# Performance work log

Measured on AMD Instinct MI355X. Metric: run time of the kernel, lower is better.

The kernel has to match this reference:

```python
import jax, jax.numpy as jnp
import numpy as np

D_MODEL = 1024
N_HEADS = 16
D_K = D_MODEL // N_HEADS
SEQ = 2048
BATCH = 2
THETA = 10000.0


def _rope(x, token_positions):
    # x: [b, h, s, dk]; token_positions: [s] int
    k = jnp.arange(0, D_K, 2, dtype=jnp.float32)
    freqs = 1.0 / (THETA ** (k / D_K))                    # [dk/2]
    angles = token_positions.astype(jnp.float32)[:, None] * freqs[None, :]  # [s, dk/2]
    cos = jnp.cos(angles)
    sin = jnp.sin(angles)
    x1 = x[..., 0::2]
    x2 = x[..., 1::2]
    r1 = x1 * cos - x2 * sin
    r2 = x1 * sin + x2 * cos
    out = jnp.stack([r1, r2], axis=-1)                    # [b,h,s,dk/2,2]
    return out.reshape(x.shape)


def setup_inputs() -> dict:
    key = jax.random.key(0)
    ks = jax.random.split(key, 5)
    sigma = np.sqrt(2.0 / (D_MODEL + D_MODEL))
    x = jax.random.normal(ks[0], (BATCH, SEQ, D_MODEL), dtype=jnp.float32)
    Wq = jax.random.truncated_normal(ks[1], -3.0, 3.0, (D_MODEL, D_MODEL), dtype=jnp.float32) * sigma
    Wk = jax.random.truncated_normal(ks[2], -3.0, 3.0, (D_MODEL, D_MODEL), dtype=jnp.float32) * sigma
    Wv = jax.random.truncated_normal(ks[3], -3.0, 3.0, (D_MODEL, D_MODEL), dtype=jnp.float32) * sigma
    Wo = jax.random.truncated_normal(ks[4], -3.0, 3.0, (D_MODEL, D_MODEL), dtype=jnp.float32) * sigma
    token_positions = jnp.arange(SEQ, dtype=jnp.int64)
    return {"x": x, "Wq": Wq, "Wk": Wk, "Wv": Wv, "Wo": Wo, "token_positions": token_positions}


def reference(x, Wq, Wk, Wv, Wo, token_positions):
    b, s, d = x.shape
    # projections: Linear stores weight [out,in], applies x @ W.T
    Q = x @ Wq.T
    K = x @ Wk.T
    V = x @ Wv.T
    # [b, s, h*dk] -> [b, h, s, dk]
    def split_heads(t):
        return t.reshape(b, s, N_HEADS, D_K).transpose(0, 2, 1, 3)
    Q, K, V = split_heads(Q), split_heads(K), split_heads(V)
    Q = _rope(Q, token_positions)
    K = _rope(K, token_positions)
    scale = 1.0 / np.sqrt(D_K).astype(np.float32)
    scores = jnp.einsum('bhqd,bhkd->bhqk', Q, K) * scale   # [b,h,s,s]
    causal = jnp.tril(jnp.ones((s, s), dtype=bool))
    scores = jnp.where(causal, scores, -jnp.inf)
    attn = jax.nn.softmax(scores, axis=-1)
    out = jnp.einsum('bhqk,bhkd->bhqd', attn, V)           # [b,h,s,dk]
    out = out.transpose(0, 2, 1, 3).reshape(b, s, d)
    return out @ Wo.T
```

## Files before the change

### kernel.cpp

```cpp
#include <hip/hip_runtime.h>
#include <hip/hip_bf16.h>
#include <stdint.h>

#define SEQL   2048
#define NBATCH 2
#define BSZ    4096
#define DMODEL 1024
#define NH     16
#define DK     64
#define NBH    32
#define NCHUNK_TOT 40

typedef __attribute__((ext_vector_type(8)))  short short8;
typedef __attribute__((ext_vector_type(4)))  short shortx4;
typedef __attribute__((ext_vector_type(4)))  float f32x4;
typedef __attribute__((ext_vector_type(16))) float f32x16;
typedef __attribute__((ext_vector_type(4)))  unsigned uint4v;
union PU { uint4v u; short8 s; };

__device__ __forceinline__ short f2b(float f) {
  unsigned u = __float_as_uint(f);
  u = (u + 0x7FFF + ((u >> 16) & 1)) >> 16;
  return (short)u;
}
__device__ __forceinline__ float b2f(short s) {
  return __uint_as_float(((unsigned)(unsigned short)s) << 16);
}
__device__ __forceinline__ unsigned cvtpk(float lo, float hi) {
  unsigned r;
  asm("v_cvt_pk_bf16_f32 %0, %1, %2" : "=v"(r) : "v"(lo), "v"(hi));
  return r;
}
__device__ __forceinline__ float max3f(float a, float b, float c) {
  float d;
  asm("v_max3_f32 %0, %1, %2, %3" : "=v"(d) : "v"(a), "v"(b), "v"(c));
  return d;
}
#define PLSWAP(a_, b_) asm("v_permlane32_swap_b32 %0, %1" : "+v"(a_), "+v"(b_))

__device__ __forceinline__ void g2l16(const void* g, void* l) {
  __builtin_amdgcn_global_load_lds(
      (__attribute__((address_space(1))) void*)(uintptr_t)g,
      (__attribute__((address_space(3))) void*)l, 16, 0, 0);
}

__device__ __forceinline__ f32x4 mfma16(short8 a, short8 b, f32x4 c) {
  return __builtin_amdgcn_mfma_f32_16x16x32_bf16(a, b, c, 0, 0, 0);
}
__device__ __forceinline__ f32x16 mfma32(short8 a, short8 b, f32x16 c) {
  return __builtin_amdgcn_mfma_f32_32x32x16_bf16(a, b, c, 0, 0, 0);
}

__global__ void cvt_all(const float* __restrict__ x,  const float* __restrict__ wq,
                        const float* __restrict__ wk, const float* __restrict__ wv,
                        const float* __restrict__ wo, short* __restrict__ xb,
                        short* __restrict__ wqkv, short* __restrict__ wob) {
  long idx = ((long)blockIdx.x * 256 + threadIdx.x) * 4;
  const float* s; short* d; long off;
  if (idx < 4194304L)      { s = x;  d = xb;             off = idx; }
  else if (idx < 5242880L) { s = wq; d = wqkv;           off = idx - 4194304L; }
  else if (idx < 6291456L) { s = wk; d = wqkv + 1048576; off = idx - 5242880L; }
  else if (idx < 7340032L) { s = wv; d = wqkv + 2097152; off = idx - 6291456L; }
  else                     { s = wo; d = wob;            off = idx - 7340032L; }
  float4 v = *(const float4*)(s + off);
  shortx4 r;
  r[0] = f2b(v.x); r[1] = f2b(v.y); r[2] = f2b(v.z); r[3] = f2b(v.w);
  *(shortx4*)(d + off) = r;
}

__global__ __launch_bounds__(512, 1)
void gemm256(const short* __restrict__ A, const short* __restrict__ B,
             short* __restrict__ C) {
  __shared__ short As[2][16384];
  __shared__ short Bs[2][12288];
  int id = blockIdx.x;
  int swz = (id & 7) * 32 + (id >> 3);
  int bm = swz >> 4, bn = swz & 15;
  int brow = bm << 8, bcoln = bn * 192;
  int tid = threadIdx.x, w = tid >> 6;
  int wm = w >> 2, wn = w & 3;
  int lr = tid & 15, lg = (tid >> 4) & 3;
  const short* Abase = A + (long)brow * 1024;
  const short* Bbase = B + (long)bcoln * 1024;

  f32x4 acc[8][3];
#pragma unroll
  for (int mi = 0; mi < 8; ++mi)
#pragma unroll
    for (int ni = 0; ni < 3; ++ni) acc[mi][ni] = (f32x4){0.f, 0.f, 0.f, 0.f};

#define STGA(s_, kt_, buf_) do {                                                \
    int r_ = tid >> 3, gch_ = (tid & 7) ^ (r_ & 7);                             \
    g2l16(Abase + (long)((s_) * 64 + r_) * 1024 + (kt_) * 64 + gch_ * 8,        \
          &As[buf_][(s_) * 4096 + tid * 8]); } while (0)
#define STGB(s_, kt_, buf_) do {                                                \
    int r_ = tid >> 3, gch_ = (tid & 7) ^ (r_ & 7);                             \
    g2l16(Bbase + (long)((s_) * 64 + r_) * 1024 + (kt_) * 64 + gch_ * 8,        \
          &Bs[buf_][(s_) * 4096 + tid * 8]); } while (0)

  STGA(0,0,0); STGA(1,0,0); STGA(2,0,0); STGA(3,0,0);
  STGB(0,0,0); STGB(1,0,0); STGB(2,0,0);
  STGA(0,1,1); STGA(1,1,1); STGA(2,1,1); STGA(3,1,1);
  STGB(0,1,1); STGB(1,1,1); STGB(2,1,1);
  asm volatile("s_waitcnt vmcnt(7)" ::: "memory");
  __builtin_amdgcn_s_barrier();

  for (int kt = 0; kt < 16; ++kt) {
    int cur = kt & 1;
    const short* Ah = &As[cur][wm * 8192];
    const short* Bh = &Bs[cur][0];
    short8 a0[4][2], a1[4][2], bf[3][2];
#pragma unroll
    for (int mi = 0; mi < 4; ++mi) {
      int rin = mi * 16 + lr;
#pragma unroll
      for (int ks = 0; ks < 2; ++ks)
        a0[mi][ks] = *(const short8*)
            &Ah[rin * 64 + (((ks * 4 + lg) ^ (rin & 7)) << 3)];
    }
#pragma unroll
    for (int ni = 0; ni < 3; ++ni) {
      int ci = wn * 48 + ni * 16 + lr;
      int sub = ci >> 6, rin = ci & 63;
#pragma unroll
      for (int ks = 0; ks < 2; ++ks)
        bf[ni][ks] = *(const short8*)
            &Bh[sub * 4096 + rin * 64 + (((ks * 4 + lg) ^ (rin & 7)) << 3)];
    }
    asm volatile("s_waitcnt lgkmcnt(0)" ::: "memory");
    __builtin_amdgcn_sched_barrier(0);
    __builtin_amdgcn_s_setprio(1);
#pragma unroll
    for (int mi = 0; mi < 4; ++mi)
#pragma unroll
      for (int ni = 0; ni < 2; ++ni)
#pragma unroll
        for (int ks = 0; ks < 2; ++ks)
          acc[mi][ni] = mfma16(a0[mi][ks], bf[ni][ks], acc[mi][ni]);
    __builtin_amdgcn_s_setprio(0);
    __builtin_amdgcn_s_barrier();
#pragma unroll
    for (int mi = 0; mi < 4; ++mi) {
      int rin = mi * 16 + lr;
#pragma unroll
      for (int ks = 0; ks < 2; ++ks)
        a1[mi][ks] = *(const short8*)
            &Ah[4096 + rin * 64 + (((ks * 4 + lg) ^ (rin & 7)) << 3)];
    }
    __builtin_amdgcn_s_setprio(1);
#pragma unroll
    for (int mi = 0; mi < 4; ++mi)
#pragma unroll
      for (int ks = 0; ks < 2; ++ks)
        acc[mi][2] = mfma16(a0[mi][ks], bf[2][ks], acc[mi][2]);
    __builtin_amdgcn_s_setprio(0);
    asm volatile("s_waitcnt lgkmcnt(0)" ::: "memory");
    __builtin_amdgcn_sched_barrier(0);
    __builtin_amdgcn_s_barrier();
    if (kt + 2 < 16) {
      STGA(0, kt + 2, cur); STGA(1, kt + 2, cur);
      STGA(2, kt + 2, cur); STGA(3, kt + 2, cur);
    }
    __builtin_amdgcn_s_setprio(1);
#pragma unroll
    for (int mi = 0; mi < 4; ++mi)
#pragma unroll
      for (int ni = 0; ni < 2; ++ni)
#pragma unroll
        for (int ks = 0; ks < 2; ++ks)
          acc[mi + 4][ni] = mfma16(a1[mi][ks], bf[ni][ks], acc[mi + 4][ni]);
    __builtin_amdgcn_s_setprio(0);
    __builtin_amdgcn_s_barrier();
    if (kt + 2 < 16) {
      STGB(0, kt + 2, cur); STGB(1, kt + 2, cur); STGB(2, kt + 2, cur);
    }
    __builtin_amdgcn_s_setprio(1);
#pragma unroll
    for (int mi = 0; mi < 4; ++mi)
#pragma unroll
      for (int ks = 0; ks < 2; ++ks)
        acc[mi + 4][2] = mfma16(a1[mi][ks], bf[2][ks], acc[mi + 4][2]);
    __builtin_amdgcn_s_setprio(0);
    if (kt + 1 < 16) {
      if (kt + 2 < 16) asm volatile("s_waitcnt vmcnt(7)" ::: "memory");
      else             asm volatile("s_waitcnt vmcnt(0)" ::: "memory");
    }
    __builtin_amdgcn_s_barrier();
  }
#undef STGA
#undef STGB

#pragma unroll
  for (int mi = 0; mi < 8; ++mi)
#pragma unroll
    for (int ni = 0; ni < 3; ++ni)
#pragma unroll
      for (int rr = 0; rr < 4; ++rr) {
        int grow = brow + wm * 128 + mi * 16 + lg * 4 + rr;
        int gcol = bcoln + wn * 48 + ni * 16 + lr;
        int mat = gcol >> 10, cin = gcol & 1023;
        C[(long)mat * 4194304 + (long)grow * 1024 + cin] = f2b(acc[mi][ni][rr]);
      }
}

template<int CBF16>
__global__ __launch_bounds__(256, 2)
void gemm_bt(const short* __restrict__ A, const short* __restrict__ B,
             void* __restrict__ Cv, int M, int N, int K,
             long bStride, long cStride) {
  __shared__ short As[2][4096];
  __shared__ short Bs[2][4096];
  B += (long)blockIdx.y * bStride;
  int nbn = N >> 7;
  int bm = blockIdx.x / nbn, bn = blockIdx.x % nbn;
  int tid = threadIdx.x, w = tid >> 6, l = tid & 63;
  int wm = w >> 1, wn = w & 1;
  int lr = l & 15, lg = l >> 4;
  int brow = bm << 7, bcol = bn << 7;

  const f32x4 fz = {0.f, 0.f, 0.f, 0.f};
  f32x4 acc[4][4];
#pragma unroll
  for (int xi = 0; xi < 4; ++xi)
#pragma unroll
    for (int yi = 0; yi < 4; ++yi) acc[xi][yi] = fz;

#define GSTAGE(k0_, bi_) do {                                                   \
    _Pragma("unroll")                                                           \
    for (int i_ = 0; i_ < 2; ++i_) {                                            \
      int c_ = w * 2 + i_;                                                      \
      int chunk_ = c_ * 64 + l;                                                 \
      int row_ = chunk_ >> 2, ch_ = chunk_ & 3;                                 \
      int gch_ = ch_ ^ ((row_ >> 1) & 3);                                       \
      g2l16(A + (long)(brow + row_) * K + (k0_) + gch_ * 8, &As[bi_][c_ * 512]);\
      g2l16(B + (long)(bcol + row_) * K + (k0_) + gch_ * 8, &Bs[bi_][c_ * 512]);\
    }                                                                           \
  } while (0)

  GSTAGE(0, 0);
  for (int k0 = 0; k0 < K; k0 += 32) {
    int cb = (k0 >> 5) & 1;
    if (k0 + 32 < K) {
      GSTAGE(k0 + 32, cb ^ 1);
      asm volatile("s_waitcnt vmcnt(4)" ::: "memory");
    } else {
      asm volatile("s_waitcnt vmcnt(0)" ::: "memory");
    }
    __builtin_amdgcn_s_barrier();

    short8 af[4], bfr[4];
#pragma unroll
    for (int xi = 0; xi < 4; ++xi) {
      int ar = wm * 64 + xi * 16 + lr;
      af[xi] = *(const short8*)&As[cb][ar * 32 + ((lg ^ ((ar >> 1) & 3)) << 3)];
      int br = wn * 64 + xi * 16 + lr;
      bfr[xi] = *(const short8*)&Bs[cb][br * 32 + ((lg ^ ((br >> 1) & 3)) << 3)];
    }
    __builtin_amdgcn_s_setprio(1);
#pragma unroll
    for (int xi = 0; xi < 4; ++xi)
#pragma unroll
      for (int yi = 0; yi < 4; ++yi)
        acc[xi][yi] = mfma16(af[xi], bfr[yi], acc[xi][yi]);
    __builtin_amdgcn_s_setprio(0);
    asm volatile("s_waitcnt lgkmcnt(0)" ::: "memory");
    __builtin_amdgcn_s_barrier();
  }
#undef GSTAGE

  if (CBF16) {
    short* Cp = (short*)Cv + (long)blockIdx.y * cStride;
#pragma unroll
    for (int xi = 0; xi < 4; ++xi)
#pragma unroll
      for (int yi = 0; yi < 4; ++yi)
#pragma unroll
        for (int r = 0; r < 4; ++r) {
          int row = brow + wm * 64 + xi * 16 + lg * 4 + r;
          int col = bcol + wn * 64 + yi * 16 + lr;
          Cp[(long)row * N + col] = f2b(acc[xi][yi][r]);
        }
  } else {
    float* Cp = (float*)Cv;
#pragma unroll
    for (int xi = 0; xi < 4; ++xi)
#pragma unroll
      for (int yi = 0; yi < 4; ++yi)
#pragma unroll
        for (int r = 0; r < 4; ++r) {
          int row = brow + wm * 64 + xi * 16 + lg * 4 + r;
          int col = bcol + wn * 64 + yi * 16 + lr;
          Cp[(long)row * N + col] = acc[xi][yi][r];
        }
  }
}

__global__ void rope_split(const short* __restrict__ qkv, const int* __restrict__ tok,
                           short* __restrict__ Qh, short* __restrict__ Kh) {
  int t = blockIdx.x * 256 + threadIdx.x;
  int qd = t & 15, h = (t >> 4) & 15, bs = t >> 8;
  int b = bs >> 11, s = bs & 2047;
  float pos = (float)tok[s];
  long srcoff = (long)bs * 1024 + h * 64 + qd * 4;
  shortx4 q4 = *(const shortx4*)(qkv + srcoff);
  shortx4 k4 = *(const shortx4*)(qkv + 4194304L + srcoff);
  shortx4 qo, ko;
#pragma unroll
  for (int p = 0; p < 2; ++p) {
    int i = qd * 2 + p;
    float freq = exp2f(-(float)i * (13.287712379549449f / 32.0f));
    float ang = pos * freq;
    float sn, cs;
    sincosf(ang, &sn, &cs);
    const float QS = 0.125f * 1.44269504f;
    float x1 = b2f(q4[p * 2]), x2 = b2f(q4[p * 2 + 1]);
    qo[p * 2]     = f2b((x1 * cs - x2 * sn) * QS);
    qo[p * 2 + 1] = f2b((x1 * sn + x2 * cs) * QS);
    float y1 = b2f(k4[p * 2]), y2 = b2f(k4[p * 2 + 1]);
    ko[p * 2]     = f2b(y1 * cs - y2 * sn);
    ko[p * 2 + 1] = f2b(y1 * sn + y2 * cs);
  }
  long outoff = ((long)(b * 16 + h) * 2048 + s) * 64 + qd * 4;
  *(shortx4*)(Qh + outoff) = qo;
  *(shortx4*)(Kh + outoff) = ko;
}

__global__ void vtrans(const short* __restrict__ Vlin, short* __restrict__ Vt) {
  __shared__ short tile[64][72];
  int s0 = blockIdx.x * 64;
  int bh = blockIdx.y;
  int b = bh >> 4, h = bh & 15;
  int t = threadIdx.x;
  int r = t >> 2, c0 = (t & 3) * 16;
  const short* src = Vlin + ((long)(b * 2048 + s0 + r)) * 1024 + h * 64 + c0;
  *(short8*)&tile[r][c0]     = *(const short8*)src;
  *(short8*)&tile[r][c0 + 8] = *(const short8*)(src + 8);
  __syncthreads();
  int d = t >> 2, sc0 = (t & 3) * 16;
  short8 o0, o1;
#pragma unroll
  for (int j = 0; j < 8; ++j) { o0[j] = tile[sc0 + j][d]; o1[j] = tile[sc0 + 8 + j][d]; }
  short* dst = Vt + ((long)(bh * 64 + d)) * 2048 + s0 + sc0;
  *(short8*)dst       = o0;
  *(short8*)(dst + 8) = o1;
}

__global__ __launch_bounds__(256, 4)
void attn_fwd(const short* __restrict__ Qh, const short* __restrict__ Kh,
              const short* __restrict__ Vt, short* __restrict__ poO,
              float* __restrict__ pmb, float* __restrict__ plb) {
  __shared__ short Ks[2][4096];
  __shared__ short Vs[2][4096];
  int bh = blockIdx.x;
  int xr = 39 - blockIdx.y;
  int qi, c = xr, nc = 1;
  for (qi = 0; qi < 16; ++qi) { nc = (qi >> 2) + 1; if (c < nc) break; c -= nc; }
  int n = 2 * qi + 2;
  int t0 = (c * n) / nc, t1 = ((c + 1) * n) / nc;
  int q0b = qi << 7;
  int tid = threadIdx.x, w = tid >> 6, l = tid & 63;
  int ql = l & 31, hi = l >> 5;
  const short* Qb = Qh + (long)bh * (2048 * 64);
  const short* Kb = Kh + (long)bh * (2048 * 64);
  const short* Vb = Vt + (long)bh * (64 * 2048);
  int qw = q0b + 32 * w;
  int qg = qw + ql;
  int pid = bh * NCHUNK_TOT + xr;

  short8 qf[4];
#pragma unroll
  for (int kc = 0; kc < 4; ++kc)
    qf[kc] = *(const short8*)(Qb + (long)qg * 64 + kc * 16 + hi * 8);

  f32x16 o0, o1, rsv;
#pragma unroll
  for (int r = 0; r < 16; ++r) { o0[r] = 0.f; o1[r] = 0.f; rsv[r] = 0.f; }
  float m = -1e30f;

#define STAGE(t_, bufi_) do {                                                   \
    int s0_ = (t_) << 6;                                                        \
    _Pragma("unroll")                                                           \
    for (int i_ = 0; i_ < 2; ++i_) {                                            \
      int c_ = w + 4 * i_;                                                      \
      int g_ = c_ >> 2, cc_ = c_ & 3;                                           \
      g2l16(Kb + ((long)(s0_ + g_ * 32 + ql)) * 64 + cc_ * 16 + hi * 8,         \
            &Ks[bufi_][c_ * 512]);                                              \
      g2l16(Vb + ((long)(g_ * 32 + ql)) * 2048 + s0_ + cc_ * 16 + hi * 8,       \
            &Vs[bufi_][c_ * 512]);                                              \
    }                                                                           \
  } while (0)

  STAGE(t0, 0);

  for (int t = t0; t < t1; ++t) {
    int cur = (t - t0) & 1;
    if (t + 1 < t1) {
      STAGE(t + 1, cur ^ 1);
      asm volatile("s_waitcnt vmcnt(4)" ::: "memory");
    } else {
      asm volatile("s_waitcnt vmcnt(0)" ::: "memory");
    }
    __builtin_amdgcn_s_barrier();
    int s0 = t << 6;
    if (s0 <= qw + 31) {
      bool upper = (s0 + 32 <= qw + 31);
      f32x16 sT0, sT1;
#pragma unroll
      for (int r = 0; r < 16; ++r) { sT0[r] = 0.f; sT1[r] = 0.f; }
      __builtin_amdgcn_s_setprio(1);
#pragma unroll
      for (int kc = 0; kc < 4; ++kc) {
        short8 k0 = *(const short8*)&Ks[cur][(kc * 64 + l) * 8];
        sT0 = mfma32(k0, qf[kc], sT0);
      }
      if (upper) {
#pragma unroll
        for (int kc = 0; kc < 4; ++kc) {
          short8 k1 = *(const short8*)&Ks[cur][((4 + kc) * 64 + l) * 8];
          sT1 = mfma32(k1, qf[kc], sT1);
        }
      }
      __builtin_amdgcn_s_setprio(0);
      if (s0 + 63 > qw) {
#pragma unroll
        for (int r = 0; r < 16; ++r) {
          int kvl = (r & 3) + 8 * (r >> 2) + 4 * hi;
          if (s0 + kvl > qg) sT0[r] = -1e30f;
        }
        if (upper) {
#pragma unroll
          for (int r = 0; r < 16; ++r) {
            int kvl = (r & 3) + 8 * (r >> 2) + 4 * hi;
            if (s0 + 32 + kvl > qg) sT1[r] = -1e30f;
          }
        }
      }
      float pmax = fmaxf(sT0[0], sT0[1]);
#pragma unroll
      for (int r = 2; r < 16; r += 2) pmax = max3f(pmax, sT0[r], sT0[r + 1]);
      if (upper) {
#pragma unroll
        for (int r = 0; r < 16; r += 2) pmax = max3f(pmax, sT1[r], sT1[r + 1]);
      }
      pmax = fmaxf(pmax, __shfl_xor(pmax, 32));
      if (__any(pmax > m + 11.5416f)) {
        float mn = fmaxf(m, pmax);
        float sf = exp2f(m - mn);
        m = mn;
#pragma unroll
        for (int r = 0; r < 16; ++r) rsv[r] *= sf;
#pragma unroll
        for (int r = 0; r < 16; ++r) {
          int row = (r & 3) + 8 * (r >> 2) + 4 * hi;
          float fo = __shfl(sf, row);
          o0[r] *= fo; o1[r] *= fo;
        }
      }
#pragma unroll
      for (int r = 0; r < 16; ++r) {
        float p = exp2f(sT0[r] - m);
        sT0[r] = p; rsv[r] += p;
      }
      if (upper) {
#pragma unroll
        for (int r = 0; r < 16; ++r) {
          float p = exp2f(sT1[r] - m);
          sT1[r] = p; rsv[r] += p;
        }
      }
      short8 pa[4];
      {
        unsigned cA[4], cB[4];
#pragma unroll
        for (int g = 0; g < 4; ++g) {
          cA[g] = cvtpk(sT0[4 * g], sT0[4 * g + 1]);
          cB[g] = cvtpk(sT0[4 * g + 2], sT0[4 * g + 3]);
        }
        PLSWAP(cA[0], cA[1]); PLSWAP(cB[0], cB[1]);
        PLSWAP(cA[2], cA[3]); PLSWAP(cB[2], cB[3]);
        PU p0; p0.u = (uint4v){cA[0], cB[0], cA[1], cB[1]}; pa[0] = p0.s;
        PU p1; p1.u = (uint4v){cA[2], cB[2], cA[3], cB[3]}; pa[1] = p1.s;
      }
      if (upper) {
        unsigned cA[4], cB[4];
#pragma unroll
        for (int g = 0; g < 4; ++g) {
          cA[g] = cvtpk(sT1[4 * g], sT1[4 * g + 1]);
          cB[g] = cvtpk(sT1[4 * g + 2], sT1[4 * g + 3]);
        }
        PLSWAP(cA[0], cA[1]); PLSWAP(cB[0], cB[1]);
        PLSWAP(cA[2], cA[3]); PLSWAP(cB[2], cB[3]);
        PU p2; p2.u = (uint4v){cA[0], cB[0], cA[1], cB[1]}; pa[2] = p2.s;
        PU p3; p3.u = (uint4v){cA[2], cB[2], cA[3], cB[3]}; pa[3] = p3.s;
      }
      __builtin_amdgcn_s_setprio(1);
#pragma unroll
      for (int kc = 0; kc < 2; ++kc) {
        short8 v0 = *(const short8*)&Vs[cur][(kc * 64 + l) * 8];
        short8 v1 = *(const short8*)&Vs[cur][((4 + kc) * 64 + l) * 8];
        o0 = mfma32(pa[kc], v0, o0);
        o1 = mfma32(pa[kc], v1, o1);
      }
      if (upper) {
#pragma unroll
        for (int kc = 2; kc < 4; ++kc) {
          short8 v0 = *(const short8*)&Vs[cur][(kc * 64 + l) * 8];
          short8 v1 = *(const short8*)&Vs[cur][((4 + kc) * 64 + l) * 8];
          o0 = mfma32(pa[kc], v0, o0);
          o1 = mfma32(pa[kc], v1, o1);
        }
      }
      __builtin_amdgcn_s_setprio(0);
    }
    asm volatile("s_waitcnt lgkmcnt(0)" ::: "memory");
    __builtin_amdgcn_s_barrier();
  }
#undef STAGE

  float lsum = 0.f;
#pragma unroll
  for (int r = 0; r < 16; ++r) lsum += rsv[r];
  lsum += __shfl_xor(lsum, 32);

  if (hi == 0) {
    pmb[pid * 128 + w * 32 + ql] = m;
    plb[pid * 128 + w * 32 + ql] = lsum;
  }
#pragma unroll
  for (int r = 0; r < 16; ++r) {
    int row = (r & 3) + 8 * (r >> 2) + 4 * hi;
    long basep = ((long)pid * 128 + w * 32 + row) * 64;
    poO[basep + ql]      = f2b(o0[r]);
    poO[basep + 32 + ql] = f2b(o1[r]);
  }
}

__global__ void attn_combine(const short* __restrict__ poO,
                             const float* __restrict__ pmb,
                             const float* __restrict__ plb,
                             short* __restrict__ Oh) {
  int x = blockIdx.x, bh = blockIdx.y;
  int qi = x >> 2, sub = x & 3;
  int t = threadIdx.x;
  int r = sub * 32 + (t >> 3);
  int d0 = (t & 7) * 8;
  int nc = (qi >> 2) + 1;
  int prefix = 0;
  for (int j = 0; j < qi; ++j) prefix += (j >> 2) + 1;
  int base = bh * NCHUNK_TOT + prefix;
  float M = -1e30f;
  for (int i = 0; i < nc; ++i)
    M = fmaxf(M, pmb[(base + i) * 128 + r]);
  float acc0 = 0, acc1 = 0, acc2 = 0, acc3 = 0, acc4 = 0, acc5 = 0, acc6 = 0, acc7 = 0;
  float den = 0.f;
  for (int i = 0; i < nc; ++i) {
    float wgt = exp2f(pmb[(base + i) * 128 + r] - M);
    den += wgt * plb[(base + i) * 128 + r];
    short8 ov = *(const short8*)&poO[((long)(base + i) * 128 + r) * 64 + d0];
    acc0 += wgt * b2f(ov[0]); acc1 += wgt * b2f(ov[1]);
    acc2 += wgt * b2f(ov[2]); acc3 += wgt * b2f(ov[3]);
    acc4 += wgt * b2f(ov[4]); acc5 += wgt * b2f(ov[5]);
    acc6 += wgt * b2f(ov[6]); acc7 += wgt * b2f(ov[7]);
  }
  float inv = 1.0f / den;
  int b = bh >> 4, h = bh & 15;
  int s = qi * 128 + r;
  short8 out;
  out[0] = f2b(acc0 * inv); out[1] = f2b(acc1 * inv);
  out[2] = f2b(acc2 * inv); out[3] = f2b(acc3 * inv);
  out[4] = f2b(acc4 * inv); out[5] = f2b(acc5 * inv);
  out[6] = f2b(acc6 * inv); out[7] = f2b(acc7 * inv);
  *(short8*)&Oh[((long)(b * 2048 + s)) * 1024 + h * 64 + d0] = out;
}

extern "C" void kernel_launch(void* const* d_in, const int* in_sizes, int n_in,
                              void* d_out, int out_size, void* d_ws, size_t ws_size,
                              hipStream_t stream) {
  const float* x  = (const float*)d_in[0];
  const float* wq = (const float*)d_in[1];
  const float* wk = (const float*)d_in[2];
  const float* wv = (const float*)d_in[3];
  const float* wo = (const float*)d_in[4];
  const int* tok  = (const int*)d_in[5];

  short* wsp  = (short*)d_ws;
  short* xb   = wsp;
  short* wqkv = xb + 4194304;
  short* wob  = wqkv + 3145728;
  short* qkv  = wob + 1048576;
  short* qh   = qkv + 12582912;
  short* kh   = qh + 4194304;
  short* vt   = kh + 4194304;
  short* oh   = vt + 4194304;

  short* poO = qkv;
  float* pmb = (float*)xb;
  float* plb = pmb + NCHUNK_TOT * NBH * 128;

  (void)in_sizes; (void)n_in; (void)out_size; (void)ws_size;

  cvt_all<<<8192, 256, 0, stream>>>(x, wq, wk, wv, wo, xb, wqkv, wob);
  gemm256<<<256, 512, 0, stream>>>(xb, wqkv, qkv);
  rope_split<<<4096, 256, 0, stream>>>(qkv, tok, qh, kh);
  vtrans<<<dim3(32, 32), 256, 0, stream>>>(qkv + 8388608, vt);
  attn_fwd<<<dim3(32, NCHUNK_TOT), 256, 0, stream>>>(qh, kh, vt, poO, pmb, plb);
  attn_combine<<<dim3(64, 32), 256, 0, stream>>>(poO, pmb, plb, oh);
  gemm_bt<0><<<dim3(256, 1), 256, 0, stream>>>(oh, wob, d_out, 4096, 1024, 1024,
                                               0L, 0L);
}
```

Before: 142.3 us.

## Fuse RoPE into QKV GEMM epilogue and triple-buffer attention K/V

Moves the RoPE rotation and Q scaling into the QKV GEMM epilogue, using lane shuffles to pair adjacent columns and hardware sin/cos on range-reduced revolutions, which removes the separate rope_split kernel and its round trip through the intermediate buffer. The attention kernel moves from double to triple buffering of K/V tiles in LDS, with occupancy lowered from 4 to 3 blocks per SM. The row-sum accumulator becomes one scalar per thread, reduced across lanes every tile instead of once at the end, and max3 is replaced by plain fmax. Risks are scattered 2-byte stores to qh/kh in the epilogue, extra transcendental work there, and lower occupancy in attention.

```diff
diff --git a/kernel.cpp b/kernel.cpp
--- a/kernel.cpp
+++ b/kernel.cpp
@@ -30,11 +30,6 @@
   unsigned r;
   asm("v_cvt_pk_bf16_f32 %0, %1, %2" : "=v"(r) : "v"(lo), "v"(hi));
   return r;
-}
-__device__ __forceinline__ float max3f(float a, float b, float c) {
-  float d;
-  asm("v_max3_f32 %0, %1, %2, %3" : "=v"(d) : "v"(a), "v"(b), "v"(c));
-  return d;
 }
 #define PLSWAP(a_, b_) asm("v_permlane32_swap_b32 %0, %1" : "+v"(a_), "+v"(b_))
 
@@ -70,7 +65,8 @@
 
 __global__ __launch_bounds__(512, 1)
 void gemm256(const short* __restrict__ A, const short* __restrict__ B,
-             short* __restrict__ C) {
+             const int* __restrict__ tok, short* __restrict__ qh,
+             short* __restrict__ kh, short* __restrict__ vlin) {
   __shared__ short As[2][16384];
   __shared__ short Bs[2][12288];
   int id = blockIdx.x;
@@ -190,17 +186,46 @@
 #undef STGA
 #undef STGB
 
-#pragma unroll
-  for (int mi = 0; mi < 8; ++mi)
-#pragma unroll
-    for (int ni = 0; ni < 3; ++ni)
-#pragma unroll
-      for (int rr = 0; rr < 4; ++rr) {
-        int grow = brow + wm * 128 + mi * 16 + lg * 4 + rr;
-        int gcol = bcoln + wn * 48 + ni * 16 + lr;
-        int mat = gcol >> 10, cin = gcol & 1023;
-        C[(long)mat * 4194304 + (long)grow * 1024 + cin] = f2b(acc[mi][ni][rr]);
-      }
+  int sbase = brow + wm * 128;
+#pragma unroll
+  for (int ni = 0; ni < 3; ++ni) {
+    int gcol = bcoln + wn * 48 + ni * 16 + lr;
+    int mat = gcol >> 10;
+    int cin = gcol & 1023;
+    if (mat == 2) {
+#pragma unroll
+      for (int mi = 0; mi < 8; ++mi)
+#pragma unroll
+        for (int rr = 0; rr < 4; ++rr) {
+          int grow = sbase + mi * 16 + lg * 4 + rr;
+          vlin[(long)grow * 1024 + cin] = f2b(acc[mi][ni][rr]);
+        }
+    } else {
+      short* dst = mat ? kh : qh;
+      float scale = mat ? 1.0f : 0.125f * 1.44269504f;
+      int d = cin & 63, h = cin >> 6;
+      int i = d >> 1;
+      int odd = d & 1;
+      float frev = exp2f(-(float)i * 0.41524101186f) * 0.15915494309f;
+#pragma unroll
+      for (int mi = 0; mi < 8; ++mi)
+#pragma unroll
+        for (int rr = 0; rr < 4; ++rr) {
+          int grow = sbase + mi * 16 + lg * 4 + rr;
+          int s = grow & 2047, b = grow >> 11;
+          float pos = (float)tok[s];
+          float rev = pos * frev;
+          float fr = rev - floorf(rev);
+          float sn, cs;
+          asm("v_sin_f32 %0, %1" : "=v"(sn) : "v"(fr));
+          asm("v_cos_f32 %0, %1" : "=v"(cs) : "v"(fr));
+          float v = acc[mi][ni][rr];
+          float p = __shfl_xor(v, 1);
+          float out = odd ? (p * sn + v * cs) : (v * cs - p * sn);
+          dst[((long)(b * 16 + h) * 2048 + s) * 64 + d] = f2b(out * scale);
+        }
+    }
+  }
 }
 
 template<int CBF16>
@@ -295,36 +320,6 @@
   }
 }
 
-__global__ void rope_split(const short* __restrict__ qkv, const int* __restrict__ tok,
-                           short* __restrict__ Qh, short* __restrict__ Kh) {
-  int t = blockIdx.x * 256 + threadIdx.x;
-  int qd = t & 15, h = (t >> 4) & 15, bs = t >> 8;
-  int b = bs >> 11, s = bs & 2047;
-  float pos = (float)tok[s];
-  long srcoff = (long)bs * 1024 + h * 64 + qd * 4;
-  shortx4 q4 = *(const shortx4*)(qkv + srcoff);
-  shortx4 k4 = *(const shortx4*)(qkv + 4194304L + srcoff);
-  shortx4 qo, ko;
-#pragma unroll
-  for (int p = 0; p < 2; ++p) {
-    int i = qd * 2 + p;
-    float freq = exp2f(-(float)i * (13.287712379549449f / 32.0f));
-    float ang = pos * freq;
-    float sn, cs;
-    sincosf(ang, &sn, &cs);
-    const float QS = 0.125f * 1.44269504f;
-    float x1 = b2f(q4[p * 2]), x2 = b2f(q4[p * 2 + 1]);
-    qo[p * 2]     = f2b((x1 * cs - x2 * sn) * QS);
-    qo[p * 2 + 1] = f2b((x1 * sn + x2 * cs) * QS);
-    float y1 = b2f(k4[p * 2]), y2 = b2f(k4[p * 2 + 1]);
-    ko[p * 2]     = f2b(y1 * cs - y2 * sn);
-    ko[p * 2 + 1] = f2b(y1 * sn + y2 * cs);
-  }
-  long outoff = ((long)(b * 16 + h) * 2048 + s) * 64 + qd * 4;
-  *(shortx4*)(Qh + outoff) = qo;
-  *(shortx4*)(Kh + outoff) = ko;
-}
-
 __global__ void vtrans(const short* __restrict__ Vlin, short* __restrict__ Vt) {
   __shared__ short tile[64][72];
   int s0 = blockIdx.x * 64;
@@ -345,12 +340,12 @@
   *(short8*)(dst + 8) = o1;
 }
 
-__global__ __launch_bounds__(256, 4)
+__global__ __launch_bounds__(256, 3)
 void attn_fwd(const short* __restrict__ Qh, const short* __restrict__ Kh,
               const short* __restrict__ Vt, short* __restrict__ poO,
               float* __restrict__ pmb, float* __restrict__ plb) {
-  __shared__ short Ks[2][4096];
-  __shared__ short Vs[2][4096];
+  __shared__ short Ks[3][4096];
+  __shared__ short Vs[3][4096];
   int bh = blockIdx.x;
   int xr = 39 - blockIdx.y;
   int qi, c = xr, nc = 1;
@@ -372,10 +367,10 @@
   for (int kc = 0; kc < 4; ++kc)
     qf[kc] = *(const short8*)(Qb + (long)qg * 64 + kc * 16 + hi * 8);
 
-  f32x16 o0, o1, rsv;
-#pragma unroll
-  for (int r = 0; r < 16; ++r) { o0[r] = 0.f; o1[r] = 0.f; rsv[r] = 0.f; }
-  float m = -1e30f;
+  f32x16 o0, o1;
+#pragma unroll
+  for (int r = 0; r < 16; ++r) { o0[r] = 0.f; o1[r] = 0.f; }
+  float m = -1e30f, lsum = 0.f;
 
 #define STAGE(t_, bufi_) do {                                                   \
     int s0_ = (t_) << 6;                                                        \
@@ -391,11 +386,15 @@
   } while (0)
 
   STAGE(t0, 0);
+  if (t0 + 1 < t1) STAGE(t0 + 1, 1);
+  int cur = 0;
 
   for (int t = t0; t < t1; ++t) {
-    int cur = (t - t0) & 1;
-    if (t + 1 < t1) {
-      STAGE(t + 1, cur ^ 1);
+    if (t + 2 < t1) {
+      int nb = cur + 2; if (nb >= 3) nb -= 3;
+      STAGE(t + 2, nb);
+      asm volatile("s_waitcnt vmcnt(8)" ::: "memory");
+    } else if (t + 1 < t1) {
       asm volatile("s_waitcnt vmcnt(4)" ::: "memory");
     } else {
       asm volatile("s_waitcnt vmcnt(0)" ::: "memory");
@@ -435,20 +434,19 @@
           }
         }
       }
-      float pmax = fmaxf(sT0[0], sT0[1]);
-#pragma unroll
-      for (int r = 2; r < 16; r += 2) pmax = max3f(pmax, sT0[r], sT0[r + 1]);
+      float pmax = sT0[0];
+#pragma unroll
+      for (int r = 1; r < 16; ++r) pmax = fmaxf(pmax, sT0[r]);
       if (upper) {
 #pragma unroll
-        for (int r = 0; r < 16; r += 2) pmax = max3f(pmax, sT1[r], sT1[r + 1]);
+        for (int r = 0; r < 16; ++r) pmax = fmaxf(pmax, sT1[r]);
       }
       pmax = fmaxf(pmax, __shfl_xor(pmax, 32));
       if (__any(pmax > m + 11.5416f)) {
         float mn = fmaxf(m, pmax);
         float sf = exp2f(m - mn);
         m = mn;
-#pragma unroll
-        for (int r = 0; r < 16; ++r) rsv[r] *= sf;
+        lsum *= sf;
 #pragma unroll
         for (int r = 0; r < 16; ++r) {
           int row = (r & 3) + 8 * (r >> 2) + 4 * hi;
@@ -456,18 +454,21 @@
           o0[r] *= fo; o1[r] *= fo;
         }
       }
+      float rs = 0.f;
 #pragma unroll
       for (int r = 0; r < 16; ++r) {
         float p = exp2f(sT0[r] - m);
-        sT0[r] = p; rsv[r] += p;
+        sT0[r] = p; rs += p;
       }
       if (upper) {
 #pragma unroll
         for (int r = 0; r < 16; ++r) {
           float p = exp2f(sT1[r] - m);
-          sT1[r] = p; rsv[r] += p;
-        }
-      }
+          sT1[r] = p; rs += p;
+        }
+      }
+      rs += __shfl_xor(rs, 32);
+      lsum += rs;
       short8 pa[4];
       {
         unsigned cA[4], cB[4];
@@ -514,13 +515,9 @@
     }
     asm volatile("s_waitcnt lgkmcnt(0)" ::: "memory");
     __builtin_amdgcn_s_barrier();
+    ++cur; if (cur >= 3) cur -= 3;
   }
 #undef STAGE
-
-  float lsum = 0.f;
-#pragma unroll
-  for (int r = 0; r < 16; ++r) lsum += rsv[r];
-  lsum += __shfl_xor(lsum, 32);
 
   if (hi == 0) {
     pmb[pid * 128 + w * 32 + ql] = m;
@@ -593,6 +590,7 @@
   short* vt   = kh + 4194304;
   short* oh   = vt + 4194304;
 
+  short* vlin = qkv + 8388608;
   short* poO = qkv;
   float* pmb = (float*)xb;
   float* plb = pmb + NCHUNK_TOT * NBH * 128;
@@ -600,9 +598,8 @@
   (void)in_sizes; (void)n_in; (void)out_size; (void)ws_size;
 
   cvt_all<<<8192, 256, 0, stream>>>(x, wq, wk, wv, wo, xb, wqkv, wob);
-  gemm256<<<256, 512, 0, stream>>>(xb, wqkv, qkv);
-  rope_split<<<4096, 256, 0, stream>>>(qkv, tok, qh, kh);
-  vtrans<<<dim3(32, 32), 256, 0, stream>>>(qkv + 8388608, vt);
+  gemm256<<<256, 512, 0, stream>>>(xb, wqkv, tok, qh, kh, vlin);
+  vtrans<<<dim3(32, 32), 256, 0, stream>>>(vlin, vt);
   attn_fwd<<<dim3(32, NCHUNK_TOT), 256, 0, stream>>>(qh, kh, vt, poO, pmb, plb);
   attn_combine<<<dim3(64, 32), 256, 0, stream>>>(poO, pmb, plb, oh);
   gemm_bt<0><<<dim3(256, 1), 256, 0, stream>>>(oh, wob, d_out, 4096, 1024, 1024,
```

Measured after the change: 124.7 us (median of 2 runs). 12.3% less time.
